# Kernel optimization log

Hardware: AMD Instinct MI355X
Metric: run time of the kernel (lower is better)

## Reference

```python
import jax, jax.numpy as jnp
import numpy as np

CUTOFF = 5.0
LOG2 = float(np.log(2.0))

def ssp(x):
    # shifted softplus: softplus(x) - log(2)
    return jax.nn.softplus(x) - LOG2

def setup_inputs() -> dict:
    key = jax.random.key(0)
    ks = jax.random.split(key, 12)
    Nb, Na, Nnbh = 8, 1024, 64
    A, F, S = 128, 128, 50
    x = jax.random.normal(ks[0], (Nb, Na, A), dtype=jnp.float32)
    r_ij = jax.random.uniform(ks[1], (Nb, Na, Nnbh), dtype=jnp.float32) * 8.0  # some beyond cutoff=5
    neighbors = jax.random.randint(ks[2], (Nb, Na, Nnbh), 0, Na)
    neighbor_mask = (jax.random.uniform(ks[3], (Nb, Na, Nnbh)) > 0.1).astype(jnp.float32)
    f_ij = jax.random.normal(ks[4], (Nb, Na, Nnbh, S), dtype=jnp.float32)
    sc = lambda n: 1.0 / np.sqrt(n)
    W_in2f = jax.random.normal(ks[5], (F, A), dtype=jnp.float32) * sc(A)
    W_f1 = jax.random.normal(ks[6], (F, S), dtype=jnp.float32) * sc(S)
    b_f1 = jnp.zeros((F,), jnp.float32)
    W_f2 = jax.random.normal(ks[7], (F, F), dtype=jnp.float32) * sc(F)
    b_f2 = jnp.zeros((F,), jnp.float32)
    W_f2out = jax.random.normal(ks[8], (A, F), dtype=jnp.float32) * sc(F)
    b_f2out = jnp.zeros((A,), jnp.float32)
    W_dense = jax.random.normal(ks[9], (A, A), dtype=jnp.float32) * sc(A)
    b_dense = jnp.zeros((A,), jnp.float32)
    return {"x": x, "r_ij": r_ij, "neighbors": neighbors, "neighbor_mask": neighbor_mask,
            "f_ij": f_ij, "W_in2f": W_in2f, "W_f1": W_f1, "b_f1": b_f1, "W_f2": W_f2,
            "b_f2": b_f2, "W_f2out": W_f2out, "b_f2out": b_f2out, "W_dense": W_dense,
            "b_dense": b_dense}

def reference(x, r_ij, neighbors, neighbor_mask, f_ij, W_in2f, W_f1, b_f1, W_f2, b_f2,
              W_f2out, b_f2out, W_dense, b_dense):
    # filter network: Dense(S->F, ssp) -> Dense(F->F)
    W = ssp(jnp.einsum('bans,fs->banf', f_ij, W_f1) + b_f1)
    W = jnp.einsum('bang,fg->banf', W, W_f2) + b_f2          # [Nb,Na,Nnbh,F]
    # hard cutoff
    C = (r_ij <= CUTOFF).astype(W.dtype)                      # [Nb,Na,Nnbh]
    W = W * C[..., None]
    # in2f (no bias)
    y = jnp.einsum('bai,fi->baf', x, W_in2f)                  # [Nb,Na,F]
    # gather neighbor features along atom axis
    yg = jax.vmap(lambda yb, nb: yb[nb])(y, neighbors)        # [Nb,Na,Nnbh,F]
    # masked sum over neighbor axis (Aggregate, mean=False)
    v = jnp.sum(yg * W * neighbor_mask[..., None], axis=2)    # [Nb,Na,F]
    # f2out: Dense(F->A) with ssp, then dense: Dense(A->A)
    v = ssp(jnp.einsum('baf,af->ba' + 'f'[0:0] + 'a'[0:0], v, W_f2out).reshape(v.shape[:2] + (W_f2out.shape[0],)) if False else ssp(v @ W_f2out.T + b_f2out))
    out = v @ W_dense.T + b_dense                             # [Nb,Na,A]
    return out
```

## Files before the change

### kernel.cpp

```cpp
#include <hip/hip_runtime.h>
#include <math.h>


#define RCUT  5.0f
#define LOG2F_ 0.69314718055994530942f

typedef __bf16 bf16x8_t __attribute__((ext_vector_type(8)));
typedef float  f32x4_t  __attribute__((ext_vector_type(4)));

static __device__ __forceinline__ float sspf(float x) {
    return fmaxf(x, 0.0f) + __logf(1.0f + __expf(-fabsf(x))) - LOG2F_;
}
static __device__ __forceinline__ unsigned pack2h(__bf16 a, __bf16 b) {
    union { __bf16 h[2]; unsigned u; } un; un.h[0] = a; un.h[1] = b; return un.u;
}
static __device__ __forceinline__ unsigned pack2f(float a, float b) {
    return pack2h((__bf16)a, (__bf16)b);
}

__global__ __launch_bounds__(256, 4) void k1_prep_kernel(
    const float* __restrict__ x, const float* __restrict__ Wf,
    float* __restrict__ yout,
    const float* __restrict__ W1, const float* __restrict__ W2,
    const float* __restrict__ Wb,
    const float* __restrict__ Wc,
    unsigned* __restrict__ prep)
{
    __shared__ __bf16 Ah[16 * 136];
    __shared__ __bf16 Al[16 * 136];

    const int t = threadIdx.x;
    const int atom0 = blockIdx.x * 16;
    const int l = t & 63, m = l & 15, q = l >> 4;
    const int w = t >> 6;
    const int f0 = 32 * w + m;
    const int f1 = f0 + 16;

    {
        int i = blockIdx.x * 256 + t;
        if (i < 4096) {
            int sw = i >> 10, ft = (i >> 9) & 1, kh = (i >> 8) & 1;
            int sl = (i >> 2) & 63, j = i & 3;
            int sq = sl >> 4, sm = sl & 15;
            int f = 32 * sw + 16 * ft + sm;
            int c = kh * 16 + 4 * sq + j;
            int k0 = 2 * c, k1 = 2 * c + 1;
            float a = (k0 < 50) ? W1[f * 50 + k0] : 0.0f;
            float b = (k1 < 50) ? W1[f * 50 + k1] : 0.0f;
            prep[i] = pack2f(a, b);
        } else if (i < 12288) {
            int s = i - 4096;
            int sw = s >> 11, ft = (s >> 10) & 1, kq = (s >> 8) & 3;
            int sl = (s >> 2) & 63, j = s & 3;
            int sq = sl >> 4, sm = sl & 15;
            int f = 32 * sw + 16 * ft + sm;
            int c = 16 * kq + 4 * sq + j;
            float2 wv = ((const float2*)W2)[f * 64 + c];
            prep[i] = pack2f(wv.x, wv.y);
        } else if (i < 45056) {
            int s = i - 12288;
            int L = s >> 14;
            int r = s & 16383;
            int hl = r >> 13;
            int e = r & 8191;
            int sw = e >> 11, ft = (e >> 10) & 1, kq = (e >> 8) & 3;
            int sl = (e >> 2) & 63, j = e & 3;
            int sq = sl >> 4, sm = sl & 15;
            int f = 32 * sw + 16 * ft + sm;
            int c = 16 * kq + 4 * sq + j;
            const float* src = L ? Wc : Wb;
            float2 wv = ((const float2*)src)[f * 64 + c];
            if (hl == 0) {
                prep[i] = pack2h((__bf16)wv.x, (__bf16)wv.y);
            } else {
                __bf16 h0 = (__bf16)wv.x, h1 = (__bf16)wv.y;
                prep[i] = pack2f(wv.x - (float)h0, wv.y - (float)h1);
            }
        }
    }

    {
        const float4* A4 = (const float4*)(x + (size_t)atom0 * 128);
        unsigned* AhU = (unsigned*)Ah;
        unsigned* AlU = (unsigned*)Al;
        #pragma unroll
        for (int r = 0; r < 2; ++r) {
            int lin4 = r * 256 + t;
            int a = lin4 >> 5, k4 = lin4 & 31;
            float4 xv = A4[lin4];
            __bf16 h0=(__bf16)xv.x, h1=(__bf16)xv.y, h2=(__bf16)xv.z, h3=(__bf16)xv.w;
            int idx = a * 68 + 2 * k4;
            AhU[idx]     = pack2h(h0, h1);
            AhU[idx + 1] = pack2h(h2, h3);
            AlU[idx]     = pack2f(xv.x - (float)h0, xv.y - (float)h1);
            AlU[idx + 1] = pack2f(xv.z - (float)h2, xv.w - (float)h3);
        }
    }
    __syncthreads();

    f32x4_t acc0 = {0.f, 0.f, 0.f, 0.f};
    f32x4_t acc1 = {0.f, 0.f, 0.f, 0.f};
    #pragma unroll
    for (int kk = 0; kk < 4; ++kk) {
        bf16x8_t ah = *(const bf16x8_t*)&Ah[m * 136 + 32 * kk + 8 * q];
        bf16x8_t al = *(const bf16x8_t*)&Al[m * 136 + 32 * kk + 8 * q];
        #pragma unroll
        for (int ftl = 0; ftl < 2; ++ftl) {
            const float* wr = Wf + (size_t)(ftl ? f1 : f0) * 128 + 32 * kk + 8 * q;
            float4 wa = *(const float4*)wr;
            float4 wb4 = *(const float4*)(wr + 4);
            float wv[8] = {wa.x, wa.y, wa.z, wa.w, wb4.x, wb4.y, wb4.z, wb4.w};
            union { __bf16 h[8]; bf16x8_t v8; } wh, wl;
            #pragma unroll
            for (int k = 0; k < 8; ++k) {
                __bf16 hi = (__bf16)wv[k];
                wh.h[k] = hi;
                wl.h[k] = (__bf16)(wv[k] - (float)hi);
            }
            f32x4_t& acc = ftl ? acc1 : acc0;
            acc = __builtin_amdgcn_mfma_f32_16x16x32_bf16(ah, wh.v8, acc, 0, 0, 0);
            acc = __builtin_amdgcn_mfma_f32_16x16x32_bf16(ah, wl.v8, acc, 0, 0, 0);
            acc = __builtin_amdgcn_mfma_f32_16x16x32_bf16(al, wh.v8, acc, 0, 0, 0);
        }
    }
    #pragma unroll
    for (int r = 0; r < 4; ++r) {
        size_t row = (size_t)(atom0 + 4 * q + r) * 128;
        yout[row + f0] = acc0[r];
        yout[row + f1] = acc1[r];
    }
}

__global__ __launch_bounds__(256, 4) void interaction_kernel(
    const float* __restrict__ rij, const int* __restrict__ nbrs,
    const float* __restrict__ mask, const float* __restrict__ fij,
    const float* __restrict__ b1, const float* __restrict__ b2,
    const unsigned* __restrict__ W1S,
    const unsigned* __restrict__ W2S,
    const float* __restrict__ y, float* __restrict__ v)
{
    __shared__ __bf16 Hh[64 * 136];
    __shared__ __bf16 Hl[64 * 136];
    __shared__ float  cb[64];
    __shared__ int    nb[64];

    const int t  = threadIdx.x;
    const int a  = blockIdx.x;
    const int bi = a >> 10;
    const int p0 = a * 64;
    const int w = t >> 6, l = t & 63, m = l & 15, q = l >> 4;
    const int f0 = 32 * w + m;
    const int f1 = f0 + 16;

    if (t < 64) {
        float r = rij[p0 + t];
        cb[t] = (r <= RCUT) ? mask[p0 + t] : 0.0f;
        nb[t] = (bi << 10) + nbrs[p0 + t];
    }

    const float bb1_0 = b1[f0], bb1_1 = b1[f1];
    const float bb2_0 = b2[f0], bb2_1 = b2[f1];

    bf16x8_t w1f00 = *(const bf16x8_t*)(W1S + ((w * 2 + 0) * 2 + 0) * 256 + l * 4);
    bf16x8_t w1f01 = *(const bf16x8_t*)(W1S + ((w * 2 + 0) * 2 + 1) * 256 + l * 4);
    bf16x8_t w1f10 = *(const bf16x8_t*)(W1S + ((w * 2 + 1) * 2 + 0) * 256 + l * 4);
    bf16x8_t w1f11 = *(const bf16x8_t*)(W1S + ((w * 2 + 1) * 2 + 1) * 256 + l * 4);

    #pragma unroll 1
    for (int mt = 0; mt < 4; ++mt) {
        const float* frow = fij + (size_t)(p0 + 16 * mt + m) * 50;
        float kv[16];
        #pragma unroll
        for (int j2 = 0; j2 < 4; ++j2) {
            float2 xv = *(const float2*)(frow + 8 * q + 2 * j2);
            kv[2 * j2] = xv.x; kv[2 * j2 + 1] = xv.y;
        }
        #pragma unroll
        for (int j2 = 0; j2 < 4; ++j2) {
            int k = 32 + 8 * q + 2 * j2;
            float2 xv = make_float2(0.f, 0.f);
            if (k < 50) xv = *(const float2*)(frow + k);
            kv[8 + 2 * j2] = xv.x; kv[9 + 2 * j2] = xv.y;
        }
        union { __bf16 h[16]; bf16x8_t v8[2]; } uh, ul;
        #pragma unroll
        for (int k = 0; k < 16; ++k) {
            __bf16 hi = (__bf16)kv[k];
            uh.h[k] = hi;
            ul.h[k] = (__bf16)(kv[k] - (float)hi);
        }
        f32x4_t acc0 = {bb1_0, bb1_0, bb1_0, bb1_0};
        f32x4_t acc1 = {bb1_1, bb1_1, bb1_1, bb1_1};
        acc0 = __builtin_amdgcn_mfma_f32_16x16x32_bf16(uh.v8[0], w1f00, acc0, 0, 0, 0);
        acc0 = __builtin_amdgcn_mfma_f32_16x16x32_bf16(ul.v8[0], w1f00, acc0, 0, 0, 0);
        acc0 = __builtin_amdgcn_mfma_f32_16x16x32_bf16(uh.v8[1], w1f01, acc0, 0, 0, 0);
        acc0 = __builtin_amdgcn_mfma_f32_16x16x32_bf16(ul.v8[1], w1f01, acc0, 0, 0, 0);
        acc1 = __builtin_amdgcn_mfma_f32_16x16x32_bf16(uh.v8[0], w1f10, acc1, 0, 0, 0);
        acc1 = __builtin_amdgcn_mfma_f32_16x16x32_bf16(ul.v8[0], w1f10, acc1, 0, 0, 0);
        acc1 = __builtin_amdgcn_mfma_f32_16x16x32_bf16(uh.v8[1], w1f11, acc1, 0, 0, 0);
        acc1 = __builtin_amdgcn_mfma_f32_16x16x32_bf16(ul.v8[1], w1f11, acc1, 0, 0, 0);
        #pragma unroll
        for (int r = 0; r < 4; ++r) {
            int n = 16 * mt + 4 * q + r;
            float h0v = sspf(acc0[r]);
            float h1v = sspf(acc1[r]);
            __bf16 hh0 = (__bf16)h0v, hh1 = (__bf16)h1v;
            Hh[n * 136 + f0] = hh0;
            Hl[n * 136 + f0] = (__bf16)(h0v - (float)hh0);
            Hh[n * 136 + f1] = hh1;
            Hl[n * 136 + f1] = (__bf16)(h1v - (float)hh1);
        }
    }
    __syncthreads();

    float pv0 = 0.0f, pv1 = 0.0f;
    #pragma unroll 1
    for (int mt = 0; mt < 4; ++mt) {
        f32x4_t acc0 = {bb2_0, bb2_0, bb2_0, bb2_0};
        f32x4_t acc1 = {bb2_1, bb2_1, bb2_1, bb2_1};
        #pragma unroll
        for (int kq = 0; kq < 4; ++kq) {
            int hoff = (16 * mt + m) * 136 + 32 * kq + 8 * q;
            bf16x8_t hh = *(const bf16x8_t*)&Hh[hoff];
            bf16x8_t hl = *(const bf16x8_t*)&Hl[hoff];
            bf16x8_t w20 = *(const bf16x8_t*)(W2S + ((w * 2 + 0) * 4 + kq) * 256 + l * 4);
            bf16x8_t w21 = *(const bf16x8_t*)(W2S + ((w * 2 + 1) * 4 + kq) * 256 + l * 4);
            acc0 = __builtin_amdgcn_mfma_f32_16x16x32_bf16(hh, w20, acc0, 0, 0, 0);
            acc0 = __builtin_amdgcn_mfma_f32_16x16x32_bf16(hl, w20, acc0, 0, 0, 0);
            acc1 = __builtin_amdgcn_mfma_f32_16x16x32_bf16(hh, w21, acc1, 0, 0, 0);
            acc1 = __builtin_amdgcn_mfma_f32_16x16x32_bf16(hl, w21, acc1, 0, 0, 0);
        }
        #pragma unroll
        for (int r = 0; r < 4; ++r) {
            int n = 16 * mt + 4 * q + r;
            float cn = cb[n];
            const float* yrow = y + (size_t)nb[n] * 128;
            pv0 = fmaf(cn * yrow[f0], acc0[r], pv0);
            pv1 = fmaf(cn * yrow[f1], acc1[r], pv1);
        }
    }
    pv0 += __shfl_xor(pv0, 16);
    pv0 += __shfl_xor(pv0, 32);
    pv1 += __shfl_xor(pv1, 16);
    pv1 += __shfl_xor(pv1, 32);
    if (l < 16) {
        v[(size_t)a * 128 + f0] = pv0;
        v[(size_t)a * 128 + f1] = pv1;
    }
}

__global__ __launch_bounds__(256, 4) void mgemm2_kernel(
    const float* A,
    const unsigned* __restrict__ W1h, const unsigned* __restrict__ W1l,
    const float* __restrict__ bias1, int nssp1,
    const unsigned* __restrict__ W2h, const unsigned* __restrict__ W2l,
    const float* __restrict__ bias2, int nssp2,
    float* C)
{
    extern __shared__ float smf[];
    __bf16* Ah = (__bf16*)smf;
    __bf16* Al = (__bf16*)(smf + 1088);
    unsigned* AhU = (unsigned*)Ah;
    unsigned* AlU = (unsigned*)Al;

    const int t = threadIdx.x;
    const int atom0 = blockIdx.x * 16;
    const int w = t >> 6, l = t & 63, m = l & 15, q = l >> 4;

    {
        const float4* A4 = (const float4*)(A + (size_t)atom0 * 128);
        #pragma unroll
        for (int r = 0; r < 2; ++r) {
            int lin4 = r * 256 + t;
            int a = lin4 >> 5, k4 = lin4 & 31;
            float4 xv = A4[lin4];
            __bf16 h0=(__bf16)xv.x, h1=(__bf16)xv.y, h2=(__bf16)xv.z, h3=(__bf16)xv.w;
            int idx = a * 68 + 2 * k4;
            AhU[idx]     = pack2h(h0, h1);
            AhU[idx + 1] = pack2h(h2, h3);
            AlU[idx]     = pack2f(xv.x - (float)h0, xv.y - (float)h1);
            AlU[idx + 1] = pack2f(xv.z - (float)h2, xv.w - (float)h3);
        }
    }
    __syncthreads();

    bf16x8_t ah[4], al[4];
    #pragma unroll
    for (int kk = 0; kk < 4; ++kk) {
        int off = m * 136 + 32 * kk + 8 * q;
        ah[kk] = *(const bf16x8_t*)&Ah[off];
        al[kk] = *(const bf16x8_t*)&Al[off];
    }
    f32x4_t acc[2];
    int fidx[2];
    #pragma unroll
    for (int ft = 0; ft < 2; ++ft) {
        fidx[ft] = 16 * (2 * w + ft) + m;
        float b = bias1 ? bias1[fidx[ft]] : 0.0f;
        acc[ft] = (f32x4_t){b, b, b, b};
    }
    #pragma unroll
    for (int ft = 0; ft < 2; ++ft) {
        #pragma unroll
        for (int kk = 0; kk < 4; ++kk) {
            int wo = ((2 * w + ft) * 4 + kk) * 256 + l * 4;
            bf16x8_t wh = *(const bf16x8_t*)(W1h + wo);
            bf16x8_t wl = *(const bf16x8_t*)(W1l + wo);
            acc[ft] = __builtin_amdgcn_mfma_f32_16x16x32_bf16(ah[kk], wh, acc[ft], 0, 0, 0);
            acc[ft] = __builtin_amdgcn_mfma_f32_16x16x32_bf16(ah[kk], wl, acc[ft], 0, 0, 0);
            acc[ft] = __builtin_amdgcn_mfma_f32_16x16x32_bf16(al[kk], wh, acc[ft], 0, 0, 0);
        }
    }
    #pragma unroll
    for (int ft = 0; ft < 2; ++ft)
        #pragma unroll
        for (int r = 0; r < 4; ++r) {
            float o = acc[ft][r];
            if (nssp1 >= 1) o = sspf(o);
            if (nssp1 >= 2) o = sspf(o);
            acc[ft][r] = o;
        }

    __syncthreads();
    #pragma unroll
    for (int ft = 0; ft < 2; ++ft)
        #pragma unroll
        for (int r = 0; r < 4; ++r) {
            float o = acc[ft][r];
            __bf16 hh = (__bf16)o;
            Ah[(4 * q + r) * 136 + fidx[ft]] = hh;
            Al[(4 * q + r) * 136 + fidx[ft]] = (__bf16)(o - (float)hh);
        }
    __syncthreads();

    #pragma unroll
    for (int kk = 0; kk < 4; ++kk) {
        int off = m * 136 + 32 * kk + 8 * q;
        ah[kk] = *(const bf16x8_t*)&Ah[off];
        al[kk] = *(const bf16x8_t*)&Al[off];
    }
    #pragma unroll
    for (int ft = 0; ft < 2; ++ft) {
        float b = bias2 ? bias2[fidx[ft]] : 0.0f;
        acc[ft] = (f32x4_t){b, b, b, b};
    }
    #pragma unroll
    for (int ft = 0; ft < 2; ++ft) {
        #pragma unroll
        for (int kk = 0; kk < 4; ++kk) {
            int wo = ((2 * w + ft) * 4 + kk) * 256 + l * 4;
            bf16x8_t wh = *(const bf16x8_t*)(W2h + wo);
            bf16x8_t wl = *(const bf16x8_t*)(W2l + wo);
            acc[ft] = __builtin_amdgcn_mfma_f32_16x16x32_bf16(ah[kk], wh, acc[ft], 0, 0, 0);
            acc[ft] = __builtin_amdgcn_mfma_f32_16x16x32_bf16(ah[kk], wl, acc[ft], 0, 0, 0);
            acc[ft] = __builtin_amdgcn_mfma_f32_16x16x32_bf16(al[kk], wh, acc[ft], 0, 0, 0);
        }
    }
    #pragma unroll
    for (int ft = 0; ft < 2; ++ft)
        #pragma unroll
        for (int r = 0; r < 4; ++r) {
            float o = acc[ft][r];
            if (nssp2 >= 1) o = sspf(o);
            if (nssp2 >= 2) o = sspf(o);
            C[(size_t)(atom0 + 4 * q + r) * 128 + fidx[ft]] = o;
        }
}

extern "C" void kernel_launch(void* const* d_in, const int* in_sizes, int n_in,
                              void* d_out, int out_size, void* d_ws, size_t ws_size,
                              hipStream_t stream) {
    const float* x        = (const float*)d_in[0];
    const float* rij      = (const float*)d_in[1];
    const int*   nbrs     = (const int*)  d_in[2];
    const float* mask     = (const float*)d_in[3];
    const float* fij      = (const float*)d_in[4];
    const float* W_in2f   = (const float*)d_in[5];
    const float* W_f1     = (const float*)d_in[6];
    const float* b_f1     = (const float*)d_in[7];
    const float* W_f2     = (const float*)d_in[8];
    const float* b_f2     = (const float*)d_in[9];
    const float* W_f2out  = (const float*)d_in[10];
    const float* b_f2out  = (const float*)d_in[11];
    const float* W_dense  = (const float*)d_in[12];
    const float* b_dense  = (const float*)d_in[13];
    float* out = (float*)d_out;

    float*    y    = (float*)d_ws;
    unsigned* prep = (unsigned*)((char*)d_ws + (4u << 20));
    const unsigned* W1S   = prep;
    const unsigned* W2S   = prep + 4096;
    const unsigned* f2o_h = prep + 12288, *f2o_l = prep + 20480;
    const unsigned* den_h = prep + 28672, *den_l = prep + 36864;

    const int MG2_LDS = 2176 * 4;

    k1_prep_kernel<<<512, 256, 0, stream>>>(
        x, W_in2f, y, W_f1, W_f2, W_f2out, W_dense, prep);
    interaction_kernel<<<8192, 256, 0, stream>>>(
        rij, nbrs, mask, fij, b_f1, b_f2, W1S, W2S, y, out);
    mgemm2_kernel<<<512, 256, MG2_LDS, stream>>>(
        out, f2o_h, f2o_l, b_f2out, 2, den_h, den_l, b_dense, 0, out);
}
```

Baseline: 262.0 us.

## Drop low-part split for f_ij in first filter GEMM and vectorize H stores

The first filter-network MFMA stage no longer splits the f_ij inputs into high and low bf16 parts, which halves the MFMA count for that stage. The operand order is swapped (weights as A, f_ij as B), so each lane's accumulator now holds four consecutive features of one neighbor row. That lets the hidden activations be written to LDS as packed 8-byte stores instead of scalar bf16 stores, and the bias is loaded as a vector to match. The trade-off is lower precision on the f_ij inputs: they are now rounded to bf16 with no residual correction, so accuracy drops.

New measurement: 272.9 us. 1.04x slower.

```diff
diff --git a/kernel.cpp b/kernel.cpp
--- a/kernel.cpp
+++ b/kernel.cpp
@@ -158,7 +158,8 @@
         nb[t] = (bi << 10) + nbrs[p0 + t];
     }
 
-    const float bb1_0 = b1[f0], bb1_1 = b1[f1];
+    const f32x4_t bA0 = *(const f32x4_t*)(b1 + 32 * w + 4 * q);
+    const f32x4_t bA1 = *(const f32x4_t*)(b1 + 32 * w + 16 + 4 * q);
     const float bb2_0 = b2[f0], bb2_1 = b2[f1];
 
     bf16x8_t w1f00 = *(const bf16x8_t*)(W1S + ((w * 2 + 0) * 2 + 0) * 256 + l * 4);
@@ -182,33 +183,32 @@
             if (k < 50) xv = *(const float2*)(frow + k);
             kv[8 + 2 * j2] = xv.x; kv[9 + 2 * j2] = xv.y;
         }
-        union { __bf16 h[16]; bf16x8_t v8[2]; } uh, ul;
-        #pragma unroll
-        for (int k = 0; k < 16; ++k) {
-            __bf16 hi = (__bf16)kv[k];
-            uh.h[k] = hi;
-            ul.h[k] = (__bf16)(kv[k] - (float)hi);
-        }
-        f32x4_t acc0 = {bb1_0, bb1_0, bb1_0, bb1_0};
-        f32x4_t acc1 = {bb1_1, bb1_1, bb1_1, bb1_1};
-        acc0 = __builtin_amdgcn_mfma_f32_16x16x32_bf16(uh.v8[0], w1f00, acc0, 0, 0, 0);
-        acc0 = __builtin_amdgcn_mfma_f32_16x16x32_bf16(ul.v8[0], w1f00, acc0, 0, 0, 0);
-        acc0 = __builtin_amdgcn_mfma_f32_16x16x32_bf16(uh.v8[1], w1f01, acc0, 0, 0, 0);
-        acc0 = __builtin_amdgcn_mfma_f32_16x16x32_bf16(ul.v8[1], w1f01, acc0, 0, 0, 0);
-        acc1 = __builtin_amdgcn_mfma_f32_16x16x32_bf16(uh.v8[0], w1f10, acc1, 0, 0, 0);
-        acc1 = __builtin_amdgcn_mfma_f32_16x16x32_bf16(ul.v8[0], w1f10, acc1, 0, 0, 0);
-        acc1 = __builtin_amdgcn_mfma_f32_16x16x32_bf16(uh.v8[1], w1f11, acc1, 0, 0, 0);
-        acc1 = __builtin_amdgcn_mfma_f32_16x16x32_bf16(ul.v8[1], w1f11, acc1, 0, 0, 0);
-        #pragma unroll
-        for (int r = 0; r < 4; ++r) {
-            int n = 16 * mt + 4 * q + r;
-            float h0v = sspf(acc0[r]);
-            float h1v = sspf(acc1[r]);
-            __bf16 hh0 = (__bf16)h0v, hh1 = (__bf16)h1v;
-            Hh[n * 136 + f0] = hh0;
-            Hl[n * 136 + f0] = (__bf16)(h0v - (float)hh0);
-            Hh[n * 136 + f1] = hh1;
-            Hl[n * 136 + f1] = (__bf16)(h1v - (float)hh1);
+        union { __bf16 h[16]; bf16x8_t v8[2]; } uh;
+        #pragma unroll
+        for (int k = 0; k < 16; ++k) uh.h[k] = (__bf16)kv[k];
+
+        f32x4_t acc0 = bA0;
+        f32x4_t acc1 = bA1;
+        acc0 = __builtin_amdgcn_mfma_f32_16x16x32_bf16(w1f00, uh.v8[0], acc0, 0, 0, 0);
+        acc0 = __builtin_amdgcn_mfma_f32_16x16x32_bf16(w1f01, uh.v8[1], acc0, 0, 0, 0);
+        acc1 = __builtin_amdgcn_mfma_f32_16x16x32_bf16(w1f10, uh.v8[0], acc1, 0, 0, 0);
+        acc1 = __builtin_amdgcn_mfma_f32_16x16x32_bf16(w1f11, uh.v8[1], acc1, 0, 0, 0);
+
+        const int n = 16 * mt + m;
+        #pragma unroll
+        for (int gt = 0; gt < 2; ++gt) {
+            const f32x4_t& acc = gt ? acc1 : acc0;
+            union { __bf16 h[4]; uint2 u; } ph, pl;
+            #pragma unroll
+            for (int r = 0; r < 4; ++r) {
+                float hv = sspf(acc[r]);
+                __bf16 hh = (__bf16)hv;
+                ph.h[r] = hh;
+                pl.h[r] = (__bf16)(hv - (float)hh);
+            }
+            int off = n * 136 + 32 * w + 16 * gt + 4 * q;
+            *(uint2*)&Hh[off] = ph.u;
+            *(uint2*)&Hl[off] = pl.u;
         }
     }
     __syncthreads();
```
